# Performance work log

Hardware: AMD Instinct MI355X
Metric: run time of the kernel (lower is better)

The kernel has to match this reference:

```python
import jax, jax.numpy as jnp
from jax import lax
import numpy as np

B, W, M, F = 8, 20, 512, 16
H = 128          # n_hidden
HALF = 64        # half_hid
K = 10           # conv out channels
LONG_K = W // 2  # dilated conv kernel


def setup_inputs() -> dict:
    key = jax.random.key(0)
    ks = jax.random.split(key, 24)
    s = 0.1  # weight scale (xavier-ish)
    return {
        "X": jax.random.normal(ks[0], (B, W, M, F), jnp.float32),
        "Y": jax.random.uniform(ks[1], (B, M), jnp.float32),
        "adj": jax.random.uniform(ks[2], (M, M), jnp.float32),
        "V": jax.random.normal(ks[3], (HALF,), jnp.float32) * s,
        "bv": jax.random.normal(ks[4], (1,), jnp.float32) * s,
        "W1": jax.random.normal(ks[5], (HALF, H), jnp.float32) * s,
        "b1": jax.random.normal(ks[6], (HALF,), jnp.float32) * s,
        "W2": jax.random.normal(ks[7], (HALF, H), jnp.float32) * s,
        "Wb": jax.random.normal(ks[8], (M, M), jnp.float32) * s,
        "wb": jax.random.normal(ks[9], (1,), jnp.float32) * s,
        "conv_w": jax.random.normal(ks[10], (K, F, W), jnp.float32) * s,
        "conv_b": jax.random.normal(ks[11], (K,), jnp.float32) * s,
        "convl_w": jax.random.normal(ks[12], (K, F, LONG_K), jnp.float32) * s,
        "convl_b": jax.random.normal(ks[13], (K,), jnp.float32) * s,
        "gru_Wih": jax.random.normal(ks[14], (3 * H, F), jnp.float32) * s,
        "gru_Whh": jax.random.normal(ks[15], (3 * H, H), jnp.float32) * s,
        "gru_bih": jax.random.normal(ks[16], (3 * H,), jnp.float32) * s,
        "gru_bhh": jax.random.normal(ks[17], (3 * H,), jnp.float32) * s,
        "gc1_W": jax.random.normal(ks[18], (3 * K, H), jnp.float32) * s,
        "gc1_b": jax.random.normal(ks[19], (H,), jnp.float32) * s,
        "gc2_W": jax.random.normal(ks[20], (H, K), jnp.float32) * s,
        "gc2_b": jax.random.normal(ks[21], (K,), jnp.float32) * s,
        "out_W": jax.random.normal(ks[22], (1, H + K), jnp.float32) * s,
        "out_b": jax.random.normal(ks[23], (1,), jnp.float32) * s,
    }


def _gru_last(xseq, Wih, Whh, bih, bhh):
    # xseq: (N, T, F) -> last hidden (N, H), PyTorch GRU gate order r,z,n
    n_hid = Whh.shape[1]
    def step(h, x_t):
        gx = x_t @ Wih.T + bih
        gh = h @ Whh.T + bhh
        xr, xz, xn = jnp.split(gx, 3, axis=-1)
        hr, hz, hn = jnp.split(gh, 3, axis=-1)
        r = jax.nn.sigmoid(xr + hr)
        z = jax.nn.sigmoid(xz + hz)
        n = jnp.tanh(xn + r * hn)
        return (1.0 - z) * n + z * h, None
    h0 = jnp.zeros((xseq.shape[0], n_hid), xseq.dtype)
    hT, _ = lax.scan(step, h0, jnp.moveaxis(xseq, 1, 0))
    return hT


def _forward(X, Y, adj, V, bv, W1, b1, W2, Wb, wb, conv_w, conv_b, convl_w,
             convl_b, gru_Wih, gru_Whh, gru_bih, gru_bhh, gc1_W, gc1_b,
             gc2_W, gc2_b, out_W, out_b):
    b, w, m, f = X.shape
    # ---- temporal branch: GRU per node ----
    x = jnp.transpose(X, (0, 2, 1, 3)).reshape(b * m, w, f)
    last_hid = _gru_last(x, gru_Wih, gru_Whh, gru_bih, gru_bhh).reshape(b, m, -1)
    out_temporal = last_hid
    # ---- attention-style adaptive adjacency ----
    # hid_rpt_m[b,i,j]=last_hid[b,j]; hid_rpt_w[b,i,j]=last_hid[b,i]
    p1 = jnp.einsum('bjh,kh->bjk', last_hid, W1)  # pairs with column index j
    p2 = jnp.einsum('bih,kh->bik', last_hid, W2)  # pairs with row index i
    pre = p1[:, None, :, :] + p2[:, :, None, :] + b1  # (b,m,m,half)
    a_mx = jnp.einsum('bijk,k->bij', jax.nn.elu(pre), V) + bv[0]
    # F.normalize(p=2, dim=1)
    nrm = jnp.sqrt(jnp.sum(a_mx * a_mx, axis=1, keepdims=True))
    a_mx = a_mx / jnp.maximum(nrm, 1e-12)
    # ---- per-node conv1d (vectorized over nodes) ----
    Xc = jnp.transpose(X, (0, 2, 3, 1)).reshape(b * m, f, w)  # (bm, f, w)
    dn = ('NCH', 'OIH', 'NCH')
    r = lax.conv_general_dilated(Xc, conv_w, (1,), 'VALID', dimension_numbers=dn)
    r = r + conv_b[None, :, None]                      # (bm, K, 1)
    rl = lax.conv_general_dilated(Xc, convl_w, (1,), 'VALID',
                                  rhs_dilation=(2,), dimension_numbers=dn)
    rl = rl + convl_b[None, :, None]                   # (bm, K, long_out)
    r_cat = jnp.concatenate([r, rl], axis=-1)          # (bm, K, 1+long_out)
    r_l = jax.nn.relu(r_cat.reshape(b, m, -1))         # (b, m, (1+long_out)*K)
    # ---- gate learned adjacency with fixed adjacency ----
    c = jax.nn.sigmoid(jnp.einsum('bij,jk->bik', a_mx, Wb) + wb[0])
    A = adj[None] * c + a_mx * (1.0 - c)               # (b,m,m)
    # ---- graph convolutions: out = A @ (x @ W) + b ----
    h1 = jax.nn.relu(jnp.einsum('bij,bjh->bih', A, r_l @ gc1_W) + gc1_b)
    out_spatial = jax.nn.relu(jnp.einsum('bij,bjh->bih', A, h1 @ gc2_W) + gc2_b)
    # ---- readout ----
    out = jnp.concatenate([out_spatial, out_temporal], axis=-1)
    out = (out @ out_W.T + out_b).squeeze(-1)          # (b, m)
    y = out.reshape(-1)
    Yf = Y.reshape(-1)
    # BCE with logits: softplus(y) - Y*y, averaged
    loss = jnp.mean(jax.nn.softplus(y) - Yf * y)
    return loss, jax.nn.sigmoid(y)


def reference(X, Y, adj, V, bv, W1, b1, W2, Wb, wb, conv_w, conv_b, convl_w,
              convl_b, gru_Wih, gru_Whh, gru_bih, gru_bhh, gc1_W, gc1_b,
              gc2_W, gc2_b, out_W, out_b):
    return _forward(X, Y, adj, V, bv, W1, b1, W2, Wb, wb, conv_w, conv_b,
                    convl_w, convl_b, gru_Wih, gru_Whh, gru_bih, gru_bhh,
                    gc1_W, gc1_b, gc2_W, gc2_b, out_W, out_b)
```

## Files before the change

kernel.cpp:

```cpp
#include <hip/hip_runtime.h>
#include <math.h>

#define Bn 8
#define Wn 20
#define Mn 512
#define Fn 16
#define Hn 128

typedef __attribute__((ext_vector_type(8))) short short8;
typedef __attribute__((ext_vector_type(4))) float f32x4;
typedef unsigned short ushort_t;

__device__ __forceinline__ float sigmoidf_(float x) {
  return 1.0f / (1.0f + __expf(-x));
}
__device__ __forceinline__ float tanhf_(float x) {
  float xx = fminf(fmaxf(x, -15.f), 15.f);
  float e = __expf(2.f * xx);
  return (e - 1.f) / (e + 1.f);
}
__device__ __forceinline__ float reluf_(float x) { return fmaxf(x, 0.f); }
__device__ __forceinline__ float eluf_(float x) {
  return (x > 0.f) ? x : (__expf(x) - 1.f);
}
__device__ __forceinline__ ushort_t bf16_rne(float v) {
  unsigned u = __float_as_uint(v);
  u += 0x7FFFu + ((u >> 16) & 1u);
  return (ushort_t)(u >> 16);
}
__device__ __forceinline__ float bf16_to_f(ushort_t b) {
  return __uint_as_float(((unsigned)b) << 16);
}
__device__ __forceinline__ void split8(const float v[8], short8& hi, short8& lo) {
#pragma unroll
  for (int j = 0; j < 8; ++j) {
    ushort_t h = bf16_rne(v[j]);
    hi[j] = (short)h;
    lo[j] = (short)bf16_rne(v[j] - bf16_to_f(h));
  }
}
__device__ __forceinline__ void load_gate_frags(
    const float* __restrict__ Whh, const float* __restrict__ Wih,
    int row, int quad, short8 fr[5][2]) {
  const float* wrow = Whh + (long)row * 128;
#pragma unroll
  for (int ks = 0; ks < 4; ++ks) {
    float v[8];
    float4 a4 = *(const float4*)&wrow[ks * 32 + quad * 8];
    float4 b4 = *(const float4*)&wrow[ks * 32 + quad * 8 + 4];
    v[0] = a4.x; v[1] = a4.y; v[2] = a4.z; v[3] = a4.w;
    v[4] = b4.x; v[5] = b4.y; v[6] = b4.z; v[7] = b4.w;
    split8(v, fr[ks][0], fr[ks][1]);
  }
  {
    float v[8] = {0.f, 0.f, 0.f, 0.f, 0.f, 0.f, 0.f, 0.f};
    if (quad < 2) {
      const float* xrow = Wih + (long)row * 16;
      float4 a4 = *(const float4*)&xrow[quad * 8];
      float4 b4 = *(const float4*)&xrow[quad * 8 + 4];
      v[0] = a4.x; v[1] = a4.y; v[2] = a4.z; v[3] = a4.w;
      v[4] = b4.x; v[5] = b4.y; v[6] = b4.z; v[7] = b4.w;
    }
    split8(v, fr[4][0], fr[4][1]);
  }
}

#define LDK 168
#define HSZ (16 * LDK)
__global__ __launch_bounds__(512, 1) void gru_kernel(
    const float* __restrict__ X, const float* __restrict__ Whh,
    const float* __restrict__ Wih, const float* __restrict__ bih,
    const float* __restrict__ bhh, const float* __restrict__ W1,
    const float* __restrict__ W2, const float* __restrict__ b1,
    float* __restrict__ last_hid, float* __restrict__ p1,
    float* __restrict__ p2, float* __restrict__ d_out) {
  const int tid = threadIdx.x;
  const int wave = tid >> 6;
  const int lane = tid & 63;
  const int quad = lane >> 4;
  const int jl = lane & 15;
  const int j0 = wave * 16;
  const int blk = blockIdx.x;
  const int b = blk >> 5;
  const int m0 = (blk & 31) * 16;

  if (blk == 0 && tid == 0) d_out[0] = 0.f;

  __shared__ __align__(16) ushort_t smem_hs[4 * HSZ];

  short8 frR[5][2], frZ[5][2], frN[5][2];
  load_gate_frags(Whh, Wih, wave * 16 + jl, quad, frR);
  load_gate_frags(Whh, Wih, 128 + wave * 16 + jl, quad, frZ);
  load_gate_frags(Whh, Wih, 256 + wave * 16 + jl, quad, frN);

  const float cr  = bih[j0 + jl] + bhh[j0 + jl];
  const float cz  = bih[128 + j0 + jl] + bhh[128 + j0 + jl];
  const float cnx = bih[256 + j0 + jl];
  const float cnh = bhh[256 + j0 + jl];

  for (int i = tid; i < 4 * HSZ; i += 512) smem_hs[i] = 0;

  const float* Xb = X + (long)b * (Wn * Mn * Fn) + (long)m0 * Fn;
  float x0 = 0.f;
  if (tid < 256) x0 = Xb[tid];
  __syncthreads();
  if (tid < 256) {
    int s = tid >> 4, f = tid & 15;
    ushort_t hb = bf16_rne(x0);
    smem_hs[0 * HSZ + s * LDK + 128 + f] = hb;
    smem_hs[2 * HSZ + s * LDK + 128 + f] = bf16_rne(x0 - bf16_to_f(hb));
  }
  __syncthreads();

  float hp[4] = {0.f, 0.f, 0.f, 0.f};

  for (int t = 0; t < Wn; ++t) {
    const int cur = t & 1, nxt = cur ^ 1;
    const int hiC = cur * HSZ, loC = (2 + cur) * HSZ;
    const int hiN = nxt * HSZ, loN = (2 + nxt) * HSZ;
    float xpre = 0.f;
    if (tid < 256 && t < Wn - 1) xpre = Xb[(long)(t + 1) * (Mn * Fn) + tid];

    f32x4 aR[2], aZ[2], aHN[2], aXN;
    aR[0] = aR[1] = aZ[0] = aZ[1] = aHN[0] = aHN[1] = aXN = (f32x4){0.f, 0.f, 0.f, 0.f};
#pragma unroll
    for (int ks = 0; ks < 5; ++ks) {
      const int p = ks & 1;
      short8 ah = *(const short8*)&smem_hs[hiC + jl * LDK + ks * 32 + quad * 8];
      short8 al = *(const short8*)&smem_hs[loC + jl * LDK + ks * 32 + quad * 8];
      aR[p] = __builtin_amdgcn_mfma_f32_16x16x32_bf16(ah, frR[ks][0], aR[p], 0, 0, 0);
      aR[p] = __builtin_amdgcn_mfma_f32_16x16x32_bf16(ah, frR[ks][1], aR[p], 0, 0, 0);
      aR[p] = __builtin_amdgcn_mfma_f32_16x16x32_bf16(al, frR[ks][0], aR[p], 0, 0, 0);
      aZ[p] = __builtin_amdgcn_mfma_f32_16x16x32_bf16(ah, frZ[ks][0], aZ[p], 0, 0, 0);
      aZ[p] = __builtin_amdgcn_mfma_f32_16x16x32_bf16(ah, frZ[ks][1], aZ[p], 0, 0, 0);
      aZ[p] = __builtin_amdgcn_mfma_f32_16x16x32_bf16(al, frZ[ks][0], aZ[p], 0, 0, 0);
      if (ks < 4) {
        aHN[p] = __builtin_amdgcn_mfma_f32_16x16x32_bf16(ah, frN[ks][0], aHN[p], 0, 0, 0);
        aHN[p] = __builtin_amdgcn_mfma_f32_16x16x32_bf16(ah, frN[ks][1], aHN[p], 0, 0, 0);
        aHN[p] = __builtin_amdgcn_mfma_f32_16x16x32_bf16(al, frN[ks][0], aHN[p], 0, 0, 0);
      } else {
        aXN = __builtin_amdgcn_mfma_f32_16x16x32_bf16(ah, frN[4][0], aXN, 0, 0, 0);
        aXN = __builtin_amdgcn_mfma_f32_16x16x32_bf16(ah, frN[4][1], aXN, 0, 0, 0);
        aXN = __builtin_amdgcn_mfma_f32_16x16x32_bf16(al, frN[4][0], aXN, 0, 0, 0);
      }
    }

#pragma unroll
    for (int reg = 0; reg < 4; ++reg) {
      float r = sigmoidf_(aR[0][reg] + aR[1][reg] + cr);
      float z = sigmoidf_(aZ[0][reg] + aZ[1][reg] + cz);
      float n = tanhf_(aXN[reg] + cnx + r * (aHN[0][reg] + aHN[1][reg] + cnh));
      float h = (1.f - z) * n + z * hp[reg];
      hp[reg] = h;
      int s = quad * 4 + reg;
      ushort_t hb = bf16_rne(h);
      smem_hs[hiN + s * LDK + j0 + jl] = hb;
      smem_hs[loN + s * LDK + j0 + jl] = bf16_rne(h - bf16_to_f(hb));
    }
    if (tid < 256 && t < Wn - 1) {
      int s = tid >> 4, f = tid & 15;
      ushort_t hb = bf16_rne(xpre);
      smem_hs[hiN + s * LDK + 128 + f] = hb;
      smem_hs[loN + s * LDK + 128 + f] = bf16_rne(xpre - bf16_to_f(hb));
    }
    __syncthreads();
  }

  float* hs_f = (float*)smem_hs;
#pragma unroll
  for (int reg = 0; reg < 4; ++reg) {
    int s = quad * 4 + reg;
    float h = hp[reg];
    last_hid[(long)(blk * 16 + s) * Hn + j0 + jl] = h;
    hs_f[s * 132 + j0 + jl] = h;
  }
  __syncthreads();
  {
    int k = tid & 63;
    int part = (tid >> 6) & 1;
    int sg = tid >> 7;
    const float* Wp = part ? W2 : W1;
    float a[4];
    float init = part ? 0.f : b1[k];
    a[0] = a[1] = a[2] = a[3] = init;
    for (int h = 0; h < 128; h += 4) {
      float4 w = *(const float4*)&Wp[k * 128 + h];
#pragma unroll
      for (int rr = 0; rr < 4; ++rr) {
        float4 q = *(const float4*)&hs_f[(sg * 4 + rr) * 132 + h];
        a[rr] += q.x * w.x + q.y * w.y + q.z * w.z + q.w * w.w;
      }
    }
    float* outp = part ? p2 : p1;
#pragma unroll
    for (int rr = 0; rr < 4; ++rr)
      outp[(long)(blk * 16 + sg * 4 + rr) * 64 + k] = a[rr];
  }
}

__global__ __launch_bounds__(256) void mid_kernel(
    const float* __restrict__ X, const float* __restrict__ conv_w,
    const float* __restrict__ conv_b, const float* __restrict__ convl_w,
    const float* __restrict__ convl_b, const float* __restrict__ gc1_W,
    const float* __restrict__ p1, const float* __restrict__ p2,
    const float* __restrict__ V, const float* __restrict__ bv,
    const float* __restrict__ Wb, ushort_t* __restrict__ t1T_hi,
    ushort_t* __restrict__ t1T_lo, ushort_t* __restrict__ WbT_hi,
    ushort_t* __restrict__ WbT_lo, float* __restrict__ amx,
    float* __restrict__ scl) {
  int tid = threadIdx.x, blk = blockIdx.x;
  __shared__ __align__(16) char sm[30720];

  {
    float* xs  = (float*)sm;
    float* cw  = (float*)(sm + 10240);
    float* clw = (float*)(sm + 23040);
    float* rs  = (float*)(sm + 29440);
    int n0 = blk * 8, b = n0 >> 9, m0 = n0 & 511;
    for (int idx = tid; idx < 3200; idx += 256) cw[idx] = conv_w[idx];
    for (int idx = tid; idx < 1600; idx += 256) clw[idx] = convl_w[idx];
    if (tid < 128) {
      for (int w = 0; w < 20; ++w)
        xs[tid * 20 + w] = X[((long)(b * 20 + w) * 512 + m0) * 16 + tid];
    }
    __syncthreads();
    if (tid < 80) {
      int s = tid / 10, k = tid % 10;
      float a0 = conv_b[k];
      float l0 = convl_b[k], l1 = convl_b[k];
      for (int f = 0; f < 16; ++f) {
        const float* xp = &xs[(s * 16 + f) * 20];
#pragma unroll
        for (int w = 0; w < 20; ++w) a0 = fmaf(xp[w], cw[k * 320 + f * 20 + w], a0);
#pragma unroll
        for (int q = 0; q < 10; ++q) {
          float wv = clw[k * 160 + f * 10 + q];
          l0 = fmaf(xp[2 * q], wv, l0);
          l1 = fmaf(xp[2 * q + 1], wv, l1);
        }
      }
      rs[s * 32 + k * 3 + 0] = reluf_(a0);
      rs[s * 32 + k * 3 + 1] = reluf_(l0);
      rs[s * 32 + k * 3 + 2] = reluf_(l1);
    }
    __syncthreads();
    if (tid < 128) {
      float w[30];
#pragma unroll
      for (int q = 0; q < 30; ++q) w[q] = gc1_W[q * 128 + tid];
      long base = ((long)b * 128 + tid) * 512 + m0;
#pragma unroll
      for (int s = 0; s < 8; ++s) {
        float a = 0.f;
#pragma unroll
        for (int q = 0; q < 30; ++q) a = fmaf(rs[s * 32 + q], w[q], a);
        ushort_t hb = bf16_rne(a);
        t1T_hi[base + s] = hb;
        t1T_lo[base + s] = bf16_rne(a - bf16_to_f(hb));
      }
    }
  }
  __syncthreads();

  {
    float* Vs   = (float*)sm;
    float* p1s  = (float*)(sm + 256);
    float* p2s  = (float*)(sm + 2432);
    float* sred = (float*)(sm + 11136);
    int j0 = (blk & 63) * 8, bz = blk >> 6;
    if (tid < 64) Vs[tid] = V[tid];
    for (int idx = tid; idx < 512; idx += 256) {
      int r = idx >> 6, k = idx & 63;
      p1s[r * 68 + k] = p1[(long)(bz * 512 + j0 + r) * 64 + k];
    }
    float bvv = bv[0];
    int r = tid >> 3, c = tid & 7;
    float ss = 0.f;
    for (int it = 0; it < 16; ++it) {
      int i0 = it * 32;
      __syncthreads();
      for (int idx = tid; idx < 2048; idx += 256) {
        int rr = idx >> 6, k = idx & 63;
        p2s[rr * 68 + k] = p2[(long)(bz * 512 + i0 + rr) * 64 + k];
      }
      __syncthreads();
      float acc = 0.f;
#pragma unroll 4
      for (int k = 0; k < 64; ++k)
        acc = fmaf(eluf_(p1s[c * 68 + k] + p2s[r * 68 + k]), Vs[k], acc);
      float v = acc + bvv;
      amx[((long)(bz * 512 + i0 + r)) * 512 + j0 + c] = v;
      ss += v * v;
    }
    sred[r * 8 + c] = ss;
    __syncthreads();
    if (tid < 8) {
      float s = 0.f;
#pragma unroll
      for (int p = 0; p < 32; ++p) s += sred[p * 8 + tid];
      scl[bz * 512 + j0 + tid] = 1.f / fmaxf(sqrtf(s), 1e-12f);
    }
  }

  if (blk < 64) {
    __syncthreads();
    float* wt = (float*)sm;
    int k0 = (blk >> 3) * 64, j0w = (blk & 7) * 64;
    for (int idx = tid; idx < 4096; idx += 256) {
      int r = idx >> 6, c = idx & 63;
      wt[r * 65 + c] = Wb[(long)(k0 + r) * 512 + j0w + c];
    }
    __syncthreads();
    for (int idx = tid; idx < 4096; idx += 256) {
      int r = idx >> 6, c = idx & 63;
      float v = wt[c * 65 + r];
      ushort_t hb = bf16_rne(v);
      WbT_hi[(long)(j0w + r) * 512 + k0 + c] = hb;
      WbT_lo[(long)(j0w + r) * 512 + k0 + c] = bf16_rne(v - bf16_to_f(hb));
    }
  }
}

#define CPK 40
__global__ __launch_bounds__(256, 2) void gemm_cA(
    const float* __restrict__ amx, const ushort_t* __restrict__ WbT_hi,
    const ushort_t* __restrict__ WbT_lo, const float* __restrict__ adj,
    const float* __restrict__ wb, const float* __restrict__ scl,
    float* __restrict__ A) {
  const int bz = blockIdx.z;
  const int i0 = blockIdx.y * 64;
  const int j0 = blockIdx.x * 64;
  const int tid = threadIdx.x;
  const int wave = tid >> 6;
  const int lane = tid & 63;
  const int quad = lane >> 4, jl = lane & 15;
  const int wm = (wave & 1) * 32, wn = (wave >> 1) * 32;

  __shared__ __align__(16) ushort_t Ahi[64][CPK];
  __shared__ __align__(16) ushort_t Alo[64][CPK];
  __shared__ __align__(16) ushort_t Bhi[64][CPK];
  __shared__ __align__(16) ushort_t Blo[64][CPK];
  __shared__ float rs_s[512];

  const float* Abase = amx + (long)bz * 262144;
  for (int i = tid; i < 512; i += 256) rs_s[i] = scl[bz * 512 + i];

  f32x4 acc[2][2];
#pragma unroll
  for (int a = 0; a < 2; ++a)
#pragma unroll
    for (int c = 0; c < 2; ++c) acc[a][c] = (f32x4){0.f, 0.f, 0.f, 0.f};

  for (int kk0 = 0; kk0 < 512; kk0 += 32) {
    __syncthreads();
#pragma unroll
    for (int l = 0; l < 2; ++l) {
      int e = l * 1024 + tid * 4;
      int r = e >> 5, kq = e & 31;
      float4 v = *(const float4*)&Abase[(long)(i0 + r) * 512 + kk0 + kq];
      float4 sc = *(const float4*)&rs_s[kk0 + kq];
      float vv[4] = {v.x * sc.x, v.y * sc.y, v.z * sc.z, v.w * sc.w};
#pragma unroll
      for (int q = 0; q < 4; ++q) {
        ushort_t hb = bf16_rne(vv[q]);
        Ahi[r][kq + q] = hb;
        Alo[r][kq + q] = bf16_rne(vv[q] - bf16_to_f(hb));
      }
    }
    {
      int r = tid >> 2, kc = (tid & 3) * 8;
      *(uint4*)&Bhi[r][kc] = *(const uint4*)&WbT_hi[(long)(j0 + r) * 512 + kk0 + kc];
      *(uint4*)&Blo[r][kc] = *(const uint4*)&WbT_lo[(long)(j0 + r) * 512 + kk0 + kc];
    }
    __syncthreads();
    short8 ah[2], al[2], bh[2], bl[2];
#pragma unroll
    for (int tm = 0; tm < 2; ++tm) {
      ah[tm] = *(const short8*)&Ahi[wm + tm * 16 + jl][quad * 8];
      al[tm] = *(const short8*)&Alo[wm + tm * 16 + jl][quad * 8];
    }
#pragma unroll
    for (int tn = 0; tn < 2; ++tn) {
      bh[tn] = *(const short8*)&Bhi[wn + tn * 16 + jl][quad * 8];
      bl[tn] = *(const short8*)&Blo[wn + tn * 16 + jl][quad * 8];
    }
#pragma unroll
    for (int tm = 0; tm < 2; ++tm)
#pragma unroll
      for (int tn = 0; tn < 2; ++tn) {
        acc[tm][tn] = __builtin_amdgcn_mfma_f32_16x16x32_bf16(ah[tm], bh[tn], acc[tm][tn], 0, 0, 0);
        acc[tm][tn] = __builtin_amdgcn_mfma_f32_16x16x32_bf16(ah[tm], bl[tn], acc[tm][tn], 0, 0, 0);
        acc[tm][tn] = __builtin_amdgcn_mfma_f32_16x16x32_bf16(al[tm], bh[tn], acc[tm][tn], 0, 0, 0);
      }
  }

  const float wbv = wb[0];
#pragma unroll
  for (int tn = 0; tn < 2; ++tn) {
    int j = j0 + wn + tn * 16 + jl;
    float sj = rs_s[j];
#pragma unroll
    for (int tm = 0; tm < 2; ++tm) {
#pragma unroll
      for (int reg = 0; reg < 4; ++reg) {
        int i = i0 + wm + tm * 16 + quad * 4 + reg;
        long ofs = (long)bz * 262144 + (long)i * 512 + j;
        float c = sigmoidf_(acc[tm][tn][reg] + wbv);
        float am = Abase[(long)i * 512 + j] * sj;
        float ad = adj[(long)i * 512 + j];
        A[ofs] = ad * c + am * (1.f - c);
      }
    }
  }
}

__global__ __launch_bounds__(512, 1) void gemm_h1t2(
    const float* __restrict__ A, const ushort_t* __restrict__ t1T_hi,
    const ushort_t* __restrict__ t1T_lo, const float* __restrict__ gc1_b,
    const float* __restrict__ gc2_W, float* __restrict__ t2) {
  const int bz = blockIdx.y;
  const int i0 = blockIdx.x * 16;
  const int tid = threadIdx.x;
  const int wave = tid >> 6;
  const int lane = tid & 63;
  const int quad = lane >> 4, jl = lane & 15;

  __shared__ __align__(16) ushort_t Ahi[16][CPK];
  __shared__ __align__(16) ushort_t Alo[16][CPK];
  __shared__ __align__(16) ushort_t Bhi[128][CPK];
  __shared__ __align__(16) ushort_t Blo[128][CPK];
  __shared__ float h1s[16][132];
  __shared__ float gw[1280];

  const float* Ab = A + (long)bz * 262144;
  for (int idx = tid; idx < 1280; idx += 512) gw[idx] = gc2_W[idx];

  f32x4 acc = {0.f, 0.f, 0.f, 0.f};

  for (int kk0 = 0; kk0 < 512; kk0 += 32) {
    __syncthreads();
    {
      int r = tid >> 5, kq = tid & 31;
      float v = Ab[(long)(i0 + r) * 512 + kk0 + kq];
      ushort_t hb = bf16_rne(v);
      Ahi[r][kq] = hb;
      Alo[r][kq] = bf16_rne(v - bf16_to_f(hb));
    }
    {
      int r = tid >> 2, kc = (tid & 3) * 8;
      *(uint4*)&Bhi[r][kc] = *(const uint4*)&t1T_hi[((long)bz * 128 + r) * 512 + kk0 + kc];
      *(uint4*)&Blo[r][kc] = *(const uint4*)&t1T_lo[((long)bz * 128 + r) * 512 + kk0 + kc];
    }
    __syncthreads();
    short8 ah = *(const short8*)&Ahi[jl][quad * 8];
    short8 al = *(const short8*)&Alo[jl][quad * 8];
    short8 bh = *(const short8*)&Bhi[wave * 16 + jl][quad * 8];
    short8 bl = *(const short8*)&Blo[wave * 16 + jl][quad * 8];
    acc = __builtin_amdgcn_mfma_f32_16x16x32_bf16(ah, bh, acc, 0, 0, 0);
    acc = __builtin_amdgcn_mfma_f32_16x16x32_bf16(ah, bl, acc, 0, 0, 0);
    acc = __builtin_amdgcn_mfma_f32_16x16x32_bf16(al, bh, acc, 0, 0, 0);
  }
  __syncthreads();
  {
    int n = wave * 16 + jl;
    float bb = gc1_b[n];
#pragma unroll
    for (int reg = 0; reg < 4; ++reg) {
      int r = quad * 4 + reg;
      h1s[r][n] = reluf_(acc[reg] + bb);
    }
  }
  __syncthreads();
  if (tid < 160) {
    int r = tid / 10, c = tid % 10;
    float a = 0.f;
#pragma unroll 4
    for (int k = 0; k < 128; ++k) a = fmaf(h1s[r][k], gw[k * 10 + c], a);
    t2[((long)bz * 512 + i0 + r) * 10 + c] = a;
  }
}

__global__ __launch_bounds__(256) void spat_readout(
    const float* __restrict__ A, const float* __restrict__ t2,
    const float* __restrict__ gc2_b, const float* __restrict__ last_hid,
    const float* __restrict__ out_W, const float* __restrict__ out_b,
    const float* __restrict__ Y, float* __restrict__ d_out) {
  int tid = threadIdx.x;
  int bz = blockIdx.y;
  int i0 = blockIdx.x * 8;
  __shared__ float t2s[5120];
  __shared__ float wS[138];
  __shared__ float osps[8][12];
  for (int idx = tid; idx < 5120; idx += 256) t2s[idx] = t2[(long)bz * 5120 + idx];
  for (int idx = tid; idx < 138; idx += 256) wS[idx] = out_W[idx];
  __syncthreads();
  int r = tid >> 5, sk = tid & 31;
  const float* Arow = A + (long)bz * 262144 + (long)(i0 + r) * 512;
  float acc[10] = {0, 0, 0, 0, 0, 0, 0, 0, 0, 0};
  for (int k = sk; k < 512; k += 32) {
    float av = Arow[k];
    const float* tp = &t2s[k * 10];
#pragma unroll
    for (int c = 0; c < 10; ++c) acc[c] = fmaf(av, tp[c], acc[c]);
  }
#pragma unroll
  for (int off = 16; off; off >>= 1)
#pragma unroll
    for (int c = 0; c < 10; ++c) acc[c] += __shfl_xor(acc[c], off);
  if (sk == 0) {
#pragma unroll
    for (int c = 0; c < 10; ++c) osps[r][c] = reluf_(acc[c] + gc2_b[c]);
  }
  __syncthreads();
  float l = 0.f;
  if (tid < 8) {
    int gid = bz * 512 + i0 + tid;
    float y = out_b[0];
#pragma unroll
    for (int k = 0; k < 10; ++k) y = fmaf(osps[tid][k], wS[k], y);
    const float* hp = &last_hid[(long)gid * 128];
    for (int h = 0; h < 128; h += 4) {
      float4 hv = *(const float4*)&hp[h];
      y = fmaf(hv.x, wS[10 + h + 0], y);
      y = fmaf(hv.y, wS[10 + h + 1], y);
      y = fmaf(hv.z, wS[10 + h + 2], y);
      y = fmaf(hv.w, wS[10 + h + 3], y);
    }
    d_out[1 + gid] = sigmoidf_(y);
    l = fmaxf(y, 0.f) + log1pf(__expf(-fabsf(y))) - Y[gid] * y;
  }
  if (tid < 64) {
#pragma unroll
    for (int off = 4; off; off >>= 1) l += __shfl_down(l, off);
    if (tid == 0) atomicAdd(d_out, l * (1.0f / 4096.f));
  }
}

extern "C" void kernel_launch(void* const* d_in, const int* in_sizes, int n_in,
                              void* d_out, int out_size, void* d_ws, size_t ws_size,
                              hipStream_t stream) {
  const float* X       = (const float*)d_in[0];
  const float* Y       = (const float*)d_in[1];
  const float* adj     = (const float*)d_in[2];
  const float* V       = (const float*)d_in[3];
  const float* bv      = (const float*)d_in[4];
  const float* W1      = (const float*)d_in[5];
  const float* b1      = (const float*)d_in[6];
  const float* W2      = (const float*)d_in[7];
  const float* Wb      = (const float*)d_in[8];
  const float* wb      = (const float*)d_in[9];
  const float* conv_w  = (const float*)d_in[10];
  const float* conv_b  = (const float*)d_in[11];
  const float* convl_w = (const float*)d_in[12];
  const float* convl_b = (const float*)d_in[13];
  const float* gWih    = (const float*)d_in[14];
  const float* gWhh    = (const float*)d_in[15];
  const float* gbih    = (const float*)d_in[16];
  const float* gbhh    = (const float*)d_in[17];
  const float* gc1_W   = (const float*)d_in[18];
  const float* gc1_b   = (const float*)d_in[19];
  const float* gc2_W   = (const float*)d_in[20];
  const float* gc2_b   = (const float*)d_in[21];
  const float* out_W   = (const float*)d_in[22];
  const float* out_b   = (const float*)d_in[23];
  float* out = (float*)d_out;

  float* ws = (float*)d_ws;
  float* lhid  = ws; ws += 524288;
  float* p1    = ws; ws += 262144;
  float* p2    = ws; ws += 262144;
  float* amx   = ws; ws += 2097152;
  float* scl   = ws; ws += 4096;
  float* Abuf  = ws; ws += 2097152;
  float* t2    = ws; ws += 40960;
  float* WbTf  = ws; ws += 262144;
  float* t1Tf  = ws; ws += 524288;
  if (ws_size < (size_t)(ws - (float*)d_ws) * sizeof(float)) return;
  ushort_t* WbT_hi = (ushort_t*)WbTf;
  ushort_t* WbT_lo = WbT_hi + 262144;
  ushort_t* t1T_hi = (ushort_t*)t1Tf;
  ushort_t* t1T_lo = t1T_hi + 524288;

  gru_kernel<<<256, 512, 0, stream>>>(X, gWhh, gWih, gbih, gbhh, W1, W2, b1,
                                      lhid, p1, p2, out);
  mid_kernel<<<512, 256, 0, stream>>>(X, conv_w, conv_b, convl_w, convl_b,
                                      gc1_W, p1, p2, V, bv, Wb,
                                      t1T_hi, t1T_lo, WbT_hi, WbT_lo, amx, scl);
  gemm_cA<<<dim3(8, 8, 8), 256, 0, stream>>>(amx, WbT_hi, WbT_lo, adj, wb,
                                             scl, Abuf);
  gemm_h1t2<<<dim3(32, 8), 512, 0, stream>>>(Abuf, t1T_hi, t1T_lo, gc1_b,
                                             gc2_W, t2);
  spat_readout<<<dim3(64, 8), 256, 0, stream>>>(Abuf, t2, gc2_b, lhid,
                                                out_W, out_b, Y, out);
}
```

Baseline: 273.3 us.

## Retile attention-score stage into 32x32 blocks with atomic column norm accumulation

The pairwise ELU attention score computation in mid_kernel is retiled from 8 columns by 512 rows per block into four 32x32 tiles per block, each thread computing a 2x2 register block with float4 shared-memory loads and V held in registers. Column sum-of-squares now goes to a global buffer through atomicAdd. That buffer is zeroed in gru_kernel, and the inverse norm is computed in gemm_cA. The aim is more operand reuse and fewer shared loads per FMA, at the cost of float atomics, which make the summation order nondeterministic. The launch-bounds hint of 2 blocks per SM is also added.

Measured after the change: 258.4 us. -5.4%, faster.

```diff
diff --git a/kernel.cpp b/kernel.cpp
--- a/kernel.cpp
+++ b/kernel.cpp
@@ -73,7 +73,8 @@
     const float* __restrict__ bhh, const float* __restrict__ W1,
     const float* __restrict__ W2, const float* __restrict__ b1,
     float* __restrict__ last_hid, float* __restrict__ p1,
-    float* __restrict__ p2, float* __restrict__ d_out) {
+    float* __restrict__ p2, float* __restrict__ ssq,
+    float* __restrict__ d_out) {
   const int tid = threadIdx.x;
   const int wave = tid >> 6;
   const int lane = tid & 63;
@@ -84,6 +85,7 @@
   const int b = blk >> 5;
   const int m0 = (blk & 31) * 16;
 
+  if (blk < 8) ssq[blk * 512 + tid] = 0.f;
   if (blk == 0 && tid == 0) d_out[0] = 0.f;
 
   __shared__ __align__(16) ushort_t smem_hs[4 * HSZ];
@@ -198,7 +200,7 @@
   }
 }
 
-__global__ __launch_bounds__(256) void mid_kernel(
+__global__ __launch_bounds__(256, 2) void mid_kernel(
     const float* __restrict__ X, const float* __restrict__ conv_w,
     const float* __restrict__ conv_b, const float* __restrict__ convl_w,
     const float* __restrict__ convl_b, const float* __restrict__ gc1_W,
@@ -207,7 +209,7 @@
     const float* __restrict__ Wb, ushort_t* __restrict__ t1T_hi,
     ushort_t* __restrict__ t1T_lo, ushort_t* __restrict__ WbT_hi,
     ushort_t* __restrict__ WbT_lo, float* __restrict__ amx,
-    float* __restrict__ scl) {
+    float* __restrict__ ssq) {
   int tid = threadIdx.x, blk = blockIdx.x;
   __shared__ __align__(16) char sm[30720];
 
@@ -260,45 +262,73 @@
       }
     }
   }
-  __syncthreads();
 
   {
-    float* Vs   = (float*)sm;
-    float* p1s  = (float*)(sm + 256);
-    float* p2s  = (float*)(sm + 2432);
-    float* sred = (float*)(sm + 11136);
-    int j0 = (blk & 63) * 8, bz = blk >> 6;
-    if (tid < 64) Vs[tid] = V[tid];
-    for (int idx = tid; idx < 512; idx += 256) {
-      int r = idx >> 6, k = idx & 63;
-      p1s[r * 68 + k] = p1[(long)(bz * 512 + j0 + r) * 64 + k];
-    }
+    float* p1s  = (float*)sm;
+    float* p2s  = (float*)(sm + 8704);
+    float* cred = (float*)(sm + 17408);
+    float4 vreg[16];
+#pragma unroll
+    for (int q = 0; q < 16; ++q) vreg[q] = *(const float4*)&V[q * 4];
     float bvv = bv[0];
-    int r = tid >> 3, c = tid & 7;
-    float ss = 0.f;
-    for (int it = 0; it < 16; ++it) {
-      int i0 = it * 32;
+    int r0 = tid >> 4, c0 = tid & 15;
+
+    for (int it = 0; it < 4; ++it) {
+      int tile = blk * 4 + it;
+      int bz = tile >> 8, ti = (tile >> 4) & 15, tj = tile & 15;
+      int i0 = ti * 32, j0 = tj * 32;
       __syncthreads();
-      for (int idx = tid; idx < 2048; idx += 256) {
-        int rr = idx >> 6, k = idx & 63;
-        p2s[rr * 68 + k] = p2[(long)(bz * 512 + i0 + rr) * 64 + k];
+      {
+        int rr = tid >> 3, cc = (tid & 7) * 8;
+        *(float4*)&p1s[rr * 68 + cc]     = *(const float4*)&p1[(long)(bz * 512 + j0 + rr) * 64 + cc];
+        *(float4*)&p1s[rr * 68 + cc + 4] = *(const float4*)&p1[(long)(bz * 512 + j0 + rr) * 64 + cc + 4];
+        *(float4*)&p2s[rr * 68 + cc]     = *(const float4*)&p2[(long)(bz * 512 + i0 + rr) * 64 + cc];
+        *(float4*)&p2s[rr * 68 + cc + 4] = *(const float4*)&p2[(long)(bz * 512 + i0 + rr) * 64 + cc + 4];
       }
       __syncthreads();
-      float acc = 0.f;
+      float acc[2][2] = {{0.f, 0.f}, {0.f, 0.f}};
 #pragma unroll 4
-      for (int k = 0; k < 64; ++k)
-        acc = fmaf(eluf_(p1s[c * 68 + k] + p2s[r * 68 + k]), Vs[k], acc);
-      float v = acc + bvv;
-      amx[((long)(bz * 512 + i0 + r)) * 512 + j0 + c] = v;
-      ss += v * v;
-    }
-    sred[r * 8 + c] = ss;
-    __syncthreads();
-    if (tid < 8) {
-      float s = 0.f;
-#pragma unroll
-      for (int p = 0; p < 32; ++p) s += sred[p * 8 + tid];
-      scl[bz * 512 + j0 + tid] = 1.f / fmaxf(sqrtf(s), 1e-12f);
+      for (int kq = 0; kq < 16; ++kq) {
+        float4 a1 = *(const float4*)&p1s[c0 * 68 + kq * 4];
+        float4 a2 = *(const float4*)&p1s[(c0 + 16) * 68 + kq * 4];
+        float4 b1 = *(const float4*)&p2s[r0 * 68 + kq * 4];
+        float4 b2 = *(const float4*)&p2s[(r0 + 16) * 68 + kq * 4];
+        float4 vv = vreg[kq];
+        acc[0][0] = fmaf(eluf_(a1.x + b1.x), vv.x, acc[0][0]);
+        acc[0][1] = fmaf(eluf_(a2.x + b1.x), vv.x, acc[0][1]);
+        acc[1][0] = fmaf(eluf_(a1.x + b2.x), vv.x, acc[1][0]);
+        acc[1][1] = fmaf(eluf_(a2.x + b2.x), vv.x, acc[1][1]);
+        acc[0][0] = fmaf(eluf_(a1.y + b1.y), vv.y, acc[0][0]);
+        acc[0][1] = fmaf(eluf_(a2.y + b1.y), vv.y, acc[0][1]);
+        acc[1][0] = fmaf(eluf_(a1.y + b2.y), vv.y, acc[1][0]);
+        acc[1][1] = fmaf(eluf_(a2.y + b2.y), vv.y, acc[1][1]);
+        acc[0][0] = fmaf(eluf_(a1.z + b1.z), vv.z, acc[0][0]);
+        acc[0][1] = fmaf(eluf_(a2.z + b1.z), vv.z, acc[0][1]);
+        acc[1][0] = fmaf(eluf_(a1.z + b2.z), vv.z, acc[1][0]);
+        acc[1][1] = fmaf(eluf_(a2.z + b2.z), vv.z, acc[1][1]);
+        acc[0][0] = fmaf(eluf_(a1.w + b1.w), vv.w, acc[0][0]);
+        acc[0][1] = fmaf(eluf_(a2.w + b1.w), vv.w, acc[0][1]);
+        acc[1][0] = fmaf(eluf_(a1.w + b2.w), vv.w, acc[1][0]);
+        acc[1][1] = fmaf(eluf_(a2.w + b2.w), vv.w, acc[1][1]);
+      }
+      float s2[2] = {0.f, 0.f};
+#pragma unroll
+      for (int aa = 0; aa < 2; ++aa)
+#pragma unroll
+        for (int cc = 0; cc < 2; ++cc) {
+          float v = acc[aa][cc] + bvv;
+          amx[((long)(bz * 512 + i0 + r0 + aa * 16)) * 512 + j0 + c0 + cc * 16] = v;
+          s2[cc] += v * v;
+        }
+      cred[r0 * 33 + c0] = s2[0];
+      cred[r0 * 33 + c0 + 16] = s2[1];
+      __syncthreads();
+      if (tid < 32) {
+        float s = 0.f;
+#pragma unroll
+        for (int p = 0; p < 16; ++p) s += cred[p * 33 + tid];
+        atomicAdd(&ssq[bz * 512 + j0 + tid], s);
+      }
     }
   }
 
@@ -325,7 +355,7 @@
 __global__ __launch_bounds__(256, 2) void gemm_cA(
     const float* __restrict__ amx, const ushort_t* __restrict__ WbT_hi,
     const ushort_t* __restrict__ WbT_lo, const float* __restrict__ adj,
-    const float* __restrict__ wb, const float* __restrict__ scl,
+    const float* __restrict__ wb, const float* __restrict__ ssq,
     float* __restrict__ A) {
   const int bz = blockIdx.z;
   const int i0 = blockIdx.y * 64;
@@ -343,7 +373,9 @@
   __shared__ float rs_s[512];
 
   const float* Abase = amx + (long)bz * 262144;
-  for (int i = tid; i < 512; i += 256) rs_s[i] = scl[bz * 512 + i];
+  const float* sb = ssq + bz * 512;
+  for (int i = tid; i < 512; i += 256)
+    rs_s[i] = 1.f / fmaxf(sqrtf(sb[i]), 1e-12f);
 
   f32x4 acc[2][2];
 #pragma unroll
@@ -570,7 +602,7 @@
   float* p1    = ws; ws += 262144;
   float* p2    = ws; ws += 262144;
   float* amx   = ws; ws += 2097152;
-  float* scl   = ws; ws += 4096;
+  float* ssq   = ws; ws += 4096;
   float* Abuf  = ws; ws += 2097152;
   float* t2    = ws; ws += 40960;
   float* WbTf  = ws; ws += 262144;
@@ -582,12 +614,12 @@
   ushort_t* t1T_lo = t1T_hi + 524288;
 
   gru_kernel<<<256, 512, 0, stream>>>(X, gWhh, gWih, gbih, gbhh, W1, W2, b1,
-                                      lhid, p1, p2, out);
+                                      lhid, p1, p2, ssq, out);
   mid_kernel<<<512, 256, 0, stream>>>(X, conv_w, conv_b, convl_w, convl_b,
                                       gc1_W, p1, p2, V, bv, Wb,
-                                      t1T_hi, t1T_lo, WbT_hi, WbT_lo, amx, scl);
+                                      t1T_hi, t1T_lo, WbT_hi, WbT_lo, amx, ssq);
   gemm_cA<<<dim3(8, 8, 8), 256, 0, stream>>>(amx, WbT_hi, WbT_lo, adj, wb,
-                                             scl, Abuf);
+                                             ssq, Abuf);
   gemm_h1t2<<<dim3(32, 8), 512, 0, stream>>>(Abuf, t1T_hi, t1T_lo, gc1_b,
                                              gc2_W, t2);
   spat_readout<<<dim3(64, 8), 256, 0, stream>>>(Abuf, t2, gc2_b, lhid,
```
